# Kernel tuning notes

Hardware: AMD Instinct MI355X
Metric: run time of the kernel (lower is better)

The kernel has to match this reference:

```python
import jax, jax.numpy as jnp
import numpy as np

# Mamba hyperparams (mamba_ssm defaults for d_model=128)
D_MODEL = 128
DEPTH = 8
D_INNER = 256   # expand=2
D_STATE = 16
D_CONV = 4
DT_RANK = 8     # ceil(D_MODEL/16)
EPS = 1e-5


def setup_inputs() -> dict:
    key = jax.random.key(0)
    ks = jax.random.split(key, 8)
    B, H, W = 1, 48, 48
    s = lambda k, shape, sc=0.02: jax.random.normal(k, shape, jnp.float32) * sc
    return {
        "x": jax.random.normal(ks[0], (B, D_MODEL, H, W), jnp.float32),
        "W_in": s(ks[1], (DEPTH, D_MODEL, 2 * D_INNER)),
        "conv_w": s(ks[2], (DEPTH, D_INNER, D_CONV), 0.2),
        "conv_b": jnp.zeros((DEPTH, D_INNER), jnp.float32),
        "W_xproj": s(ks[3], (DEPTH, D_INNER, DT_RANK + 2 * D_STATE)),
        "W_dt": s(ks[4], (DEPTH, DT_RANK, D_INNER), 0.1),
        "b_dt": jnp.full((DEPTH, D_INNER), -4.6, jnp.float32),  # softplus ~= 0.01
        "A_log": jnp.broadcast_to(
            jnp.log(jnp.arange(1, D_STATE + 1, dtype=jnp.float32)),
            (DEPTH, D_INNER, D_STATE)).copy(),
        "D_skip": jnp.ones((DEPTH, D_INNER), jnp.float32),
        "W_out": s(ks[5], (DEPTH, D_INNER, D_MODEL)),
        "rms_w": jnp.ones((DEPTH, D_MODEL), jnp.float32),
    }


def _rmsnorm(x, w):
    return x * jax.lax.rsqrt(jnp.mean(x * x, axis=-1, keepdims=True) + EPS) * w


def _mamba_layer(x, Wi, cw, cb, Wx, Wdt, bdt, Alog, Dp, Wo):
    # x: [B, L, D_MODEL]
    B, L, _ = x.shape
    xz = x @ Wi                                   # [B, L, 2*d_inner]
    xi, z = jnp.split(xz, 2, axis=-1)
    # causal depthwise conv1d, kernel D_CONV
    xp = jnp.pad(xi, ((0, 0), (D_CONV - 1, 0), (0, 0)))
    xc = sum(xp[:, k:k + L, :] * cw[:, k] for k in range(D_CONV)) + cb
    xc = jax.nn.silu(xc)                          # [B, L, d_inner]
    dbl = xc @ Wx                                 # [B, L, dt_rank + 2*d_state]
    dt_r = dbl[..., :DT_RANK]
    Bs = dbl[..., DT_RANK:DT_RANK + D_STATE]      # [B, L, d_state]
    Cs = dbl[..., DT_RANK + D_STATE:]
    dt = jax.nn.softplus(dt_r @ Wdt + bdt)        # [B, L, d_inner]
    A = -jnp.exp(Alog)                            # [d_inner, d_state]
    dA = jnp.exp(dt[..., None] * A)               # [B, L, d_inner, d_state]
    dBx = (dt * xc)[..., None] * Bs[:, :, None, :]
    # linear recurrence h_t = dA_t * h_{t-1} + dBx_t via parallel scan
    def comb(l, r):
        al, bl = l
        ar, br = r
        return ar * al, ar * bl + br
    _, h = jax.lax.associative_scan(comb, (dA, dBx), axis=1)
    y = jnp.einsum('blds,bls->bld', h, Cs) + Dp * xc
    y = y * jax.nn.silu(z)
    return y @ Wo                                 # [B, L, D_MODEL]


def reference(x, W_in, conv_w, conv_b, W_xproj, W_dt, b_dt, A_log, D_skip, W_out, rms_w):
    B, C, H, W = x.shape
    seq = x.reshape(B, C, H * W).transpose(0, 2, 1)  # [B, L, C]
    for l in range(DEPTH):
        seq = _mamba_layer(seq, W_in[l], conv_w[l], conv_b[l], W_xproj[l],
                           W_dt[l], b_dt[l], A_log[l], D_skip[l], W_out[l])
        seq = _rmsnorm(seq, rms_w[l])
    return seq.reshape(B, H, W, C).transpose(0, 3, 1, 2)
```

## Files before the change

kernel.cpp:

```cpp
#include <hip/hip_runtime.h>
#include <math.h>

#define LSEQ 2304
#define DM 128
#define DI 256
#define DS 16
#define RK 8
#define NCH 576
#define CLEN 4
#define NG 24
#define GS 24
#define NSI (DI*DS)
#define EPSF 1e-5f

__device__ __forceinline__ float silu_f(float s) { return s / (1.f + __expf(-s)); }
__device__ __forceinline__ float softplus_f(float x) { return (x > 20.f) ? x : log1pf(__expf(x)); }

template<bool FIRST>
__global__ __launch_bounds__(256, 2)
void k_head(const float* __restrict__ seq, const float* __restrict__ x0,
            const float* __restrict__ Wi,
            const float* __restrict__ cw, const float* __restrict__ cbias,
            const float* __restrict__ Wx,
            const float* __restrict__ Wdt, const float* __restrict__ bdt,
            const float* __restrict__ Alog,
            float* __restrict__ xc_g, float* __restrict__ sz_g,
            float* __restrict__ dbl_g, float* __restrict__ dt_g,
            float* __restrict__ P, float* __restrict__ S) {
    __shared__ float As[7 * 128];
    __shared__ float xcs[CLEN * 256];
    __shared__ float dtrs[CLEN * 8];
    __shared__ float dbls[CLEN * 32];
    const int c = blockIdx.x;
    const int l0 = c * CLEN;
    const int tid = threadIdx.x;
    const int d = tid;

    for (int idx = tid; idx < 7 * 128; idx += 256) {
        const int r = idx >> 7, cc = idx & 127;
        const int l = l0 - 3 + r;
        As[idx] = (l >= 0) ? (FIRST ? x0[cc * LSEQ + l] : seq[l * DM + cc]) : 0.f;
    }
    __syncthreads();

    float ax[7] = {0.f, 0.f, 0.f, 0.f, 0.f, 0.f, 0.f};
    float az[4] = {0.f, 0.f, 0.f, 0.f};
#pragma unroll 4
    for (int k = 0; k < DM; ++k) {
        const float bx = Wi[k * 512 + d];
        const float bz = Wi[k * 512 + 256 + d];
#pragma unroll
        for (int r = 0; r < 7; ++r) ax[r] += As[r * 128 + k] * bx;
#pragma unroll
        for (int r = 0; r < 4; ++r) az[r] += As[(r + 3) * 128 + k] * bz;
    }

    const float w0 = cw[d * 4 + 0], w1 = cw[d * 4 + 1];
    const float w2 = cw[d * 4 + 2], w3 = cw[d * 4 + 3];
    const float cbv = cbias[d];
    float xcv[CLEN];
#pragma unroll
    for (int r = 0; r < CLEN; ++r) {
        const float v = silu_f(cbv + w0 * ax[r] + w1 * ax[r + 1] +
                               w2 * ax[r + 2] + w3 * ax[r + 3]);
        xcv[r] = v;
        xcs[r * 256 + d] = v;
        xc_g[(l0 + r) * DI + d] = v;
        sz_g[(l0 + r) * DI + d] = silu_f(az[r]);
    }
    __syncthreads();

    if (tid < CLEN * 40) {
        const int r = tid / 40, j = tid - r * 40;
        const float* xr = &xcs[r * 256];
        float acc = 0.f;
#pragma unroll 4
        for (int k = 0; k < DI; ++k) acc += xr[k] * Wx[k * 40 + j];
        if (j < RK) dtrs[r * 8 + j] = acc;
        else {
            dbls[r * 32 + (j - 8)] = acc;
            dbl_g[(l0 + r) * 32 + (j - 8)] = acc;
        }
    }
    __syncthreads();

    float dtv[CLEN];
    {
        float wdt[8];
#pragma unroll
        for (int q = 0; q < 8; ++q) wdt[q] = Wdt[q * DI + d];
        const float bdv = bdt[d];
#pragma unroll
        for (int r = 0; r < CLEN; ++r) {
            float acc = bdv;
#pragma unroll
            for (int q = 0; q < 8; ++q) acc += dtrs[r * 8 + q] * wdt[q];
            dtv[r] = softplus_f(acc);
            dt_g[(l0 + r) * DI + d] = dtv[r];
        }
    }

    float A[16], pr[16], hs[16];
#pragma unroll
    for (int v = 0; v < 4; ++v) {
        const float4 a4 = *(const float4*)&Alog[d * DS + v * 4];
        A[v * 4 + 0] = -__expf(a4.x);
        A[v * 4 + 1] = -__expf(a4.y);
        A[v * 4 + 2] = -__expf(a4.z);
        A[v * 4 + 3] = -__expf(a4.w);
    }
#pragma unroll
    for (int s = 0; s < 16; ++s) { pr[s] = 1.f; hs[s] = 0.f; }
#pragma unroll
    for (int t = 0; t < CLEN; ++t) {
        const float dtt = dtv[t];
        const float uv = dtt * xcv[t];
        const float* Brow = &dbls[t * 32];
#pragma unroll
        for (int s = 0; s < 16; ++s) {
            const float e = __expf(dtt * A[s]);
            pr[s] *= e;
            hs[s] = e * hs[s] + uv * Brow[s];
        }
    }
    const int base = c * NSI + d * DS;
#pragma unroll
    for (int v = 0; v < 4; ++v) {
        *(float4*)&P[base + v * 4] =
            make_float4(pr[v * 4], pr[v * 4 + 1], pr[v * 4 + 2], pr[v * 4 + 3]);
        *(float4*)&S[base + v * 4] =
            make_float4(hs[v * 4], hs[v * 4 + 1], hs[v * 4 + 2], hs[v * 4 + 3]);
    }
}

__global__ __launch_bounds__(256, 4)
void k_carry1(float* __restrict__ P, float* __restrict__ S,
              float* __restrict__ Pg, float* __restrict__ Sg) {
    const int g = blockIdx.x;
    const int i = blockIdx.y * 256 + threadIdx.x;
    float G = 0.f, Pp = 1.f;
    const int base = g * GS * NSI + i;
#pragma unroll 8
    for (int k = 0; k < GS; ++k) {
        const int idx = base + k * NSI;
        const float p = P[idx];
        const float s = S[idx];
        S[idx] = G;
        P[idx] = Pp;
        G = p * G + s;
        Pp *= p;
    }
    Pg[g * NSI + i] = Pp;
    Sg[g * NSI + i] = G;
}

__global__ __launch_bounds__(256, 4)
void k_carry2(const float* __restrict__ Pg, float* __restrict__ Sg) {
    const int i = blockIdx.x * 256 + threadIdx.x;
    float G = 0.f;
#pragma unroll 8
    for (int g = 0; g < NG; ++g) {
        const int idx = g * NSI + i;
        const float p = Pg[idx];
        const float s = Sg[idx];
        Sg[idx] = G;
        G = p * G + s;
    }
}

template<bool LAST>
__global__ __launch_bounds__(256, 2)
void k_tail(const float* __restrict__ dt_g, const float* __restrict__ xc_g,
            const float* __restrict__ dbl_g, const float* __restrict__ Alog,
            const float* __restrict__ Sloc, const float* __restrict__ Ppre,
            const float* __restrict__ Gc, const float* __restrict__ Dp,
            const float* __restrict__ sz_g, const float* __restrict__ Wo,
            const float* __restrict__ rmsw, float* __restrict__ seq,
            float* __restrict__ out) {
    __shared__ float dbls[CLEN * 32];
    __shared__ float Ys[CLEN * 256];
    __shared__ float Os[CLEN * 129];
    __shared__ float red[CLEN * 32];
    __shared__ float scaleS[CLEN];
    const int c = blockIdx.x;
    const int g = c / GS;
    const int l0 = c * CLEN;
    const int tid = threadIdx.x;
    const int d = tid;

    if (tid < CLEN * 32) dbls[tid] = dbl_g[l0 * 32 + tid];

    float A[16], h[16];
#pragma unroll
    for (int v = 0; v < 4; ++v) {
        const float4 a4 = *(const float4*)&Alog[d * DS + v * 4];
        A[v * 4 + 0] = -__expf(a4.x);
        A[v * 4 + 1] = -__expf(a4.y);
        A[v * 4 + 2] = -__expf(a4.z);
        A[v * 4 + 3] = -__expf(a4.w);
        const float4 s4 = *(const float4*)&Sloc[c * NSI + d * DS + v * 4];
        const float4 p4 = *(const float4*)&Ppre[c * NSI + d * DS + v * 4];
        const float4 g4 = *(const float4*)&Gc[g * NSI + d * DS + v * 4];
        h[v * 4 + 0] = s4.x + p4.x * g4.x;
        h[v * 4 + 1] = s4.y + p4.y * g4.y;
        h[v * 4 + 2] = s4.z + p4.z * g4.z;
        h[v * 4 + 3] = s4.w + p4.w * g4.w;
    }
    float dtv[CLEN], xcv[CLEN], szv[CLEN];
#pragma unroll
    for (int r = 0; r < CLEN; ++r) {
        dtv[r] = dt_g[(l0 + r) * DI + d];
        xcv[r] = xc_g[(l0 + r) * DI + d];
        szv[r] = sz_g[(l0 + r) * DI + d];
    }
    const float dskip = Dp[d];
    __syncthreads();
#pragma unroll
    for (int t = 0; t < CLEN; ++t) {
        const float dtt = dtv[t];
        const float uv = dtt * xcv[t];
        float sum = 0.f;
#pragma unroll
        for (int s = 0; s < 16; ++s) {
            const float e = __expf(dtt * A[s]);
            h[s] = e * h[s] + uv * dbls[t * 32 + s];
            sum += h[s] * dbls[t * 32 + 16 + s];
        }
        Ys[t * 256 + d] = (sum + dskip * xcv[t]) * szv[t];
    }
    __syncthreads();

    {
        const int cc = tid & 127;
        const int kg = tid >> 7;
        const int k0 = kg * 128;
        float acc[CLEN] = {0.f, 0.f, 0.f, 0.f};
#pragma unroll 4
        for (int k = k0; k < k0 + 128; ++k) {
            const float w = Wo[k * DM + cc];
#pragma unroll
            for (int r = 0; r < CLEN; ++r) acc[r] += Ys[r * 256 + k] * w;
        }
        if (kg == 0) {
#pragma unroll
            for (int r = 0; r < CLEN; ++r) Os[r * 129 + cc] = acc[r];
        }
        __syncthreads();
        if (kg == 1) {
#pragma unroll
            for (int r = 0; r < CLEN; ++r) Os[r * 129 + cc] += acc[r];
        }
        __syncthreads();
    }

    if (tid < CLEN * 32) {
        const int r = tid >> 5, part = tid & 31;
        float ss = 0.f;
#pragma unroll
        for (int i = 0; i < 4; ++i) {
            const float v = Os[r * 129 + part * 4 + i];
            ss += v * v;
        }
        red[tid] = ss;
    }
    __syncthreads();
    if (tid < CLEN) {
        float ss = 0.f;
#pragma unroll
        for (int p = 0; p < 32; ++p) ss += red[tid * 32 + p];
        scaleS[tid] = rsqrtf(ss * (1.f / DM) + EPSF);
    }
    __syncthreads();
    if (LAST) {
        for (int idx = tid; idx < CLEN * DM; idx += 256) {
            const int r = idx >> 7, cc = idx & 127;
            out[cc * LSEQ + (l0 + r)] = Os[r * 129 + cc] * scaleS[r] * rmsw[cc];
        }
    } else {
        for (int idx = tid; idx < CLEN * DM; idx += 256) {
            const int r = idx >> 7, cc = idx & 127;
            seq[(l0 + r) * DM + cc] = Os[r * 129 + cc] * scaleS[r] * rmsw[cc];
        }
    }
}

extern "C" void kernel_launch(void* const* d_in, const int* in_sizes, int n_in,
                              void* d_out, int out_size, void* d_ws, size_t ws_size,
                              hipStream_t stream) {
    const float* x    = (const float*)d_in[0];
    const float* W_in = (const float*)d_in[1];
    const float* cw   = (const float*)d_in[2];
    const float* cb   = (const float*)d_in[3];
    const float* Wx   = (const float*)d_in[4];
    const float* Wdt  = (const float*)d_in[5];
    const float* bdt  = (const float*)d_in[6];
    const float* Alog = (const float*)d_in[7];
    const float* Dp   = (const float*)d_in[8];
    const float* Wo   = (const float*)d_in[9];
    const float* rmsw = (const float*)d_in[10];
    float* out = (float*)d_out;

    float* ws   = (float*)d_ws;
    float* seq  = ws; ws += LSEQ * DM;
    float* szb  = ws; ws += LSEQ * DI;
    float* xcb  = ws; ws += LSEQ * DI;
    float* dtb  = ws; ws += LSEQ * DI;
    float* dblb = ws; ws += LSEQ * 32;
    float* Pb   = ws; ws += NCH * NSI;
    float* Sb   = ws; ws += NCH * NSI;
    float* Pgb  = ws; ws += NG * NSI;
    float* Sgb  = ws; ws += NG * NSI;

    for (int layer = 0; layer < 8; ++layer) {
        const float* Wi_l   = W_in + (size_t)layer * DM * 512;
        const float* cw_l   = cw   + (size_t)layer * DI * 4;
        const float* cb_l   = cb   + (size_t)layer * DI;
        const float* Wx_l   = Wx   + (size_t)layer * DI * 40;
        const float* Wdt_l  = Wdt  + (size_t)layer * RK * DI;
        const float* bdt_l  = bdt  + (size_t)layer * DI;
        const float* Alog_l = Alog + (size_t)layer * DI * DS;
        const float* Dp_l   = Dp   + (size_t)layer * DI;
        const float* Wo_l   = Wo   + (size_t)layer * DI * DM;
        const float* rmsw_l = rmsw + (size_t)layer * DM;

        if (layer == 0)
            k_head<true><<<NCH, 256, 0, stream>>>(seq, x, Wi_l, cw_l, cb_l, Wx_l,
                                                  Wdt_l, bdt_l, Alog_l,
                                                  xcb, szb, dblb, dtb, Pb, Sb);
        else
            k_head<false><<<NCH, 256, 0, stream>>>(seq, x, Wi_l, cw_l, cb_l, Wx_l,
                                                   Wdt_l, bdt_l, Alog_l,
                                                   xcb, szb, dblb, dtb, Pb, Sb);

        k_carry1<<<dim3(NG, 16), 256, 0, stream>>>(Pb, Sb, Pgb, Sgb);
        k_carry2<<<16, 256, 0, stream>>>(Pgb, Sgb);

        if (layer == 7)
            k_tail<true><<<NCH, 256, 0, stream>>>(dtb, xcb, dblb, Alog_l, Sb, Pb,
                                                  Sgb, Dp_l, szb, Wo_l, rmsw_l,
                                                  seq, out);
        else
            k_tail<false><<<NCH, 256, 0, stream>>>(dtb, xcb, dblb, Alog_l, Sb, Pb,
                                                   Sgb, Dp_l, szb, Wo_l, rmsw_l,
                                                   seq, out);
    }
}
```

Baseline: 661.6 us.

## Split head kernel into input-projection kernel and scan-prep kernel

The fused head kernel is split in two. A new k_in kernel computes the input projection, causal conv and silu gates over a 288x4 grid, with each block handling 8 rows and one half of either the x or z channels, reading shared memory as float4. A second kernel, k_mid2, reloads xc from global memory and does the x-projection, dt and chunk-scan prep. This adds one launch per layer and a round trip of xc through global memory, in exchange for more parallelism and fewer redundant halo rows in the GEMM.

```diff
diff --git a/kernel.cpp b/kernel.cpp
--- a/kernel.cpp
+++ b/kernel.cpp
@@ -17,17 +17,74 @@
 __device__ __forceinline__ float softplus_f(float x) { return (x > 20.f) ? x : log1pf(__expf(x)); }
 
 template<bool FIRST>
+__global__ __launch_bounds__(256, 4)
+void k_in(const float* __restrict__ seq, const float* __restrict__ x0,
+          const float* __restrict__ Wi,
+          const float* __restrict__ cw, const float* __restrict__ cbias,
+          float* __restrict__ xc_g, float* __restrict__ sz_g) {
+    __shared__ float As[11 * 128];
+    const int l0 = blockIdx.x * 8;
+    const int half = blockIdx.y & 1;
+    const bool isZ = blockIdx.y >= 2;
+    const int tid = threadIdx.x;
+
+    for (int idx = tid; idx < 11 * 128; idx += 256) {
+        const int r = idx >> 7, cc = idx & 127;
+        const int l = l0 - 3 + r;
+        As[idx] = (l >= 0) ? (FIRST ? x0[cc * LSEQ + l] : seq[l * DM + cc]) : 0.f;
+    }
+    __syncthreads();
+
+    const int c = tid & 127;
+    const int rg = tid >> 7;
+    const int d = half * 128 + c;
+
+    if (!isZ) {
+        float ax[7] = {0.f, 0.f, 0.f, 0.f, 0.f, 0.f, 0.f};
+        for (int k4 = 0; k4 < 32; ++k4) {
+            float bv[4];
+#pragma unroll
+            for (int u = 0; u < 4; ++u) bv[u] = Wi[(k4 * 4 + u) * 512 + d];
+#pragma unroll
+            for (int r = 0; r < 7; ++r) {
+                const float4 a4 = *(const float4*)&As[(rg * 4 + r) * 128 + k4 * 4];
+                ax[r] += a4.x * bv[0] + a4.y * bv[1] + a4.z * bv[2] + a4.w * bv[3];
+            }
+        }
+        const float w0 = cw[d * 4 + 0], w1 = cw[d * 4 + 1];
+        const float w2 = cw[d * 4 + 2], w3 = cw[d * 4 + 3];
+        const float cbv = cbias[d];
+#pragma unroll
+        for (int rr = 0; rr < 4; ++rr) {
+            const float v = silu_f(cbv + w0 * ax[rr] + w1 * ax[rr + 1] +
+                                   w2 * ax[rr + 2] + w3 * ax[rr + 3]);
+            xc_g[(l0 + rg * 4 + rr) * DI + d] = v;
+        }
+    } else {
+        float az[4] = {0.f, 0.f, 0.f, 0.f};
+        for (int k4 = 0; k4 < 32; ++k4) {
+            float bv[4];
+#pragma unroll
+            for (int u = 0; u < 4; ++u) bv[u] = Wi[(k4 * 4 + u) * 512 + 256 + d];
+#pragma unroll
+            for (int r = 0; r < 4; ++r) {
+                const float4 a4 = *(const float4*)&As[(rg * 4 + r + 3) * 128 + k4 * 4];
+                az[r] += a4.x * bv[0] + a4.y * bv[1] + a4.z * bv[2] + a4.w * bv[3];
+            }
+        }
+#pragma unroll
+        for (int rr = 0; rr < 4; ++rr)
+            sz_g[(l0 + rg * 4 + rr) * DI + d] = silu_f(az[rr]);
+    }
+}
+
 __global__ __launch_bounds__(256, 2)
-void k_head(const float* __restrict__ seq, const float* __restrict__ x0,
-            const float* __restrict__ Wi,
-            const float* __restrict__ cw, const float* __restrict__ cbias,
+void k_mid2(const float* __restrict__ xc_g,
             const float* __restrict__ Wx,
             const float* __restrict__ Wdt, const float* __restrict__ bdt,
             const float* __restrict__ Alog,
-            float* __restrict__ xc_g, float* __restrict__ sz_g,
             float* __restrict__ dbl_g, float* __restrict__ dt_g,
             float* __restrict__ P, float* __restrict__ S) {
-    __shared__ float As[7 * 128];
     __shared__ float xcs[CLEN * 256];
     __shared__ float dtrs[CLEN * 8];
     __shared__ float dbls[CLEN * 32];
@@ -36,45 +93,14 @@
     const int tid = threadIdx.x;
     const int d = tid;
 
-    for (int idx = tid; idx < 7 * 128; idx += 256) {
-        const int r = idx >> 7, cc = idx & 127;
-        const int l = l0 - 3 + r;
-        As[idx] = (l >= 0) ? (FIRST ? x0[cc * LSEQ + l] : seq[l * DM + cc]) : 0.f;
-    }
-    __syncthreads();
-
-    float ax[7] = {0.f, 0.f, 0.f, 0.f, 0.f, 0.f, 0.f};
-    float az[4] = {0.f, 0.f, 0.f, 0.f};
-#pragma unroll 4
-    for (int k = 0; k < DM; ++k) {
-        const float bx = Wi[k * 512 + d];
-        const float bz = Wi[k * 512 + 256 + d];
-#pragma unroll
-        for (int r = 0; r < 7; ++r) ax[r] += As[r * 128 + k] * bx;
-#pragma unroll
-        for (int r = 0; r < 4; ++r) az[r] += As[(r + 3) * 128 + k] * bz;
-    }
-
-    const float w0 = cw[d * 4 + 0], w1 = cw[d * 4 + 1];
-    const float w2 = cw[d * 4 + 2], w3 = cw[d * 4 + 3];
-    const float cbv = cbias[d];
-    float xcv[CLEN];
-#pragma unroll
-    for (int r = 0; r < CLEN; ++r) {
-        const float v = silu_f(cbv + w0 * ax[r] + w1 * ax[r + 1] +
-                               w2 * ax[r + 2] + w3 * ax[r + 3]);
-        xcv[r] = v;
-        xcs[r * 256 + d] = v;
-        xc_g[(l0 + r) * DI + d] = v;
-        sz_g[(l0 + r) * DI + d] = silu_f(az[r]);
-    }
+    ((float4*)xcs)[tid] = ((const float4*)&xc_g[l0 * DI])[tid];
     __syncthreads();
 
     if (tid < CLEN * 40) {
         const int r = tid / 40, j = tid - r * 40;
         const float* xr = &xcs[r * 256];
         float acc = 0.f;
-#pragma unroll 4
+#pragma unroll 8
         for (int k = 0; k < DI; ++k) acc += xr[k] * Wx[k * 40 + j];
         if (j < RK) dtrs[r * 8 + j] = acc;
         else {
@@ -84,7 +110,7 @@
     }
     __syncthreads();
 
-    float dtv[CLEN];
+    float dtv[CLEN], xcv[CLEN];
     {
         float wdt[8];
 #pragma unroll
@@ -97,6 +123,7 @@
             for (int q = 0; q < 8; ++q) acc += dtrs[r * 8 + q] * wdt[q];
             dtv[r] = softplus_f(acc);
             dt_g[(l0 + r) * DI + d] = dtv[r];
+            xcv[r] = xcs[r * 256 + d];
         }
     }
 
@@ -324,13 +351,14 @@
         const float* rmsw_l = rmsw + (size_t)layer * DM;
 
         if (layer == 0)
-            k_head<true><<<NCH, 256, 0, stream>>>(seq, x, Wi_l, cw_l, cb_l, Wx_l,
-                                                  Wdt_l, bdt_l, Alog_l,
-                                                  xcb, szb, dblb, dtb, Pb, Sb);
+            k_in<true><<<dim3(288, 4), 256, 0, stream>>>(seq, x, Wi_l, cw_l, cb_l,
+                                                         xcb, szb);
         else
-            k_head<false><<<NCH, 256, 0, stream>>>(seq, x, Wi_l, cw_l, cb_l, Wx_l,
-                                                   Wdt_l, bdt_l, Alog_l,
-                                                   xcb, szb, dblb, dtb, Pb, Sb);
+            k_in<false><<<dim3(288, 4), 256, 0, stream>>>(seq, x, Wi_l, cw_l, cb_l,
+                                                          xcb, szb);
+
+        k_mid2<<<NCH, 256, 0, stream>>>(xcb, Wx_l, Wdt_l, bdt_l, Alog_l,
+                                        dblb, dtb, Pb, Sb);
 
         k_carry1<<<dim3(NG, 16), 256, 0, stream>>>(Pb, Sb, Pgb, Sgb);
         k_carry2<<<16, 256, 0, stream>>>(Pgb, Sgb);
```

After: 631.6 us. 1.05x faster.
